# Kernel tuning notes

Hardware: AMD Instinct MI355X
Metric: run time of the kernel (lower is better)

## Reference

```python
import jax, jax.numpy as jnp
import numpy as np

N_NODES = 50000
N_EDGES = 640000
N_GRAPHS = 256
H = 128
L = 4
X_DIM, P_DIM, E_DIM = 64, 16, 16


def setup_inputs() -> dict:
    key = jax.random.key(0)
    ks = jax.random.split(key, 16)
    s = 0.05
    inp = {
        "x": jax.random.normal(ks[0], (N_NODES, X_DIM), jnp.float32),
        "p": jax.random.normal(ks[1], (N_NODES, P_DIM), jnp.float32),
        "e_attr": jax.random.normal(ks[2], (N_EDGES, E_DIM), jnp.float32),
        "edge_index": jax.random.randint(ks[3], (2, N_EDGES), 0, N_NODES, jnp.int32),
        "batch": jnp.sort(jax.random.randint(ks[4], (N_NODES,), 0, N_GRAPHS, jnp.int32)),
        # embeddings
        "W_embed": jax.random.normal(ks[5], (X_DIM + P_DIM, H), jnp.float32) * s,
        "b_embed": jnp.zeros((H,), jnp.float32),
        "W_eembed": jax.random.normal(ks[6], (E_DIM, H), jnp.float32) * s,
        "b_eembed": jnp.zeros((H,), jnp.float32),
        # per-layer stacked params
        "Wm": jax.random.normal(ks[7], (L, 3 * H, H), jnp.float32) * s,
        "bm": jnp.zeros((L, H), jnp.float32),
        "Wh": jax.random.normal(ks[8], (L, 2 * H, H), jnp.float32) * s,
        "bh": jnp.zeros((L, H), jnp.float32),
        "We": jax.random.normal(ks[9], (L, 3 * H, H), jnp.float32) * s,
        "be": jnp.zeros((L, H), jnp.float32),
    }
    return inp


def reference(x, p, e_attr, W_embed, b_embed, W_eembed, b_eembed,
              Wm, bm, Wh, bh, We, be, edge_index, batch):
    # node embed: Linear(cat(x, p))
    h = jnp.concatenate([x, p], axis=1) @ W_embed + b_embed          # [N, H]
    e = e_attr @ W_eembed + b_eembed                                 # [E, H]
    send, rec = edge_index[0], edge_index[1]
    n_nodes = x.shape[0]
    for l in range(Wm.shape[0]):
        h_send, h_rec = h[send], h[rec]                              # gathers [E, H]
        cat_ser = jnp.concatenate([h_send, h_rec, e], axis=1)        # [E, 3H]
        messages = cat_ser @ Wm[l] + bm[l]                           # [E, H]
        messages_agg = jax.ops.segment_sum(messages, rec, num_segments=n_nodes)  # scatter_add
        h = jnp.concatenate([h, messages_agg], axis=1) @ Wh[l] + bh[l]
        # e_update uses h_send/h_rec gathered from the PRE-update h (as in torch code)
        e = cat_ser @ We[l] + be[l]
    # global_add_pool over graphs
    out = jax.ops.segment_sum(h, batch, num_segments=N_GRAPHS)       # [G, H]
    return out
```

## Files before the change

### kernel.cpp

```cpp
#include <hip/hip_runtime.h>
#include <cstdio>

#define NN 50000
#define NE 640000
#define NG 256
#define NL 4

#define SCAN_CHUNK 1024
#define NB_SCAN ((NN + SCAN_CHUNK - 1) / SCAN_CHUNK)

typedef unsigned short u16;
typedef unsigned int u32;
typedef __attribute__((ext_vector_type(8))) short short8v;
typedef __attribute__((ext_vector_type(4))) float f32x4;

static __device__ __forceinline__ float bf2f(u16 v) {
    return __uint_as_float(((u32)v) << 16);
}
static __device__ __forceinline__ u16 f2bf(float f) {
    u32 u = __float_as_uint(f);
    u += 0x7fff + ((u >> 16) & 1);
    return (u16)(u >> 16);
}
static __device__ __forceinline__ void gload_lds16(const u16* g, u16* l) {
    __builtin_amdgcn_global_load_lds(
        (const __attribute__((address_space(1))) u32*)g,
        (__attribute__((address_space(3))) u32*)l, 16, 0, 0);
}

__global__ __launch_bounds__(256) void k_deg(
    const int* __restrict__ rec, int* __restrict__ deg)
{
    const int e = blockIdx.x * 256 + threadIdx.x;
    atomicAdd(&deg[rec[e]], 1);
}

__global__ __launch_bounds__(256) void k_prep_xp(
    const float* __restrict__ x, const float* __restrict__ p,
    u16* __restrict__ Axp)
{
    const int idx = blockIdx.x * 256 + threadIdx.x;
    const int row = idx / 48;
    const int c2 = idx - row * 48;
    const int c0 = c2 * 2;
    float f0, f1;
    if (c0 < 64)      { f0 = x[(size_t)row * 64 + c0]; f1 = x[(size_t)row * 64 + c0 + 1]; }
    else if (c0 < 80) { f0 = p[(size_t)row * 16 + c0 - 64]; f1 = p[(size_t)row * 16 + c0 - 63]; }
    else              { f0 = 0.f; f1 = 0.f; }
    ((u32*)Axp)[idx] = (u32)f2bf(f0) | ((u32)f2bf(f1) << 16);
}

__global__ __launch_bounds__(256) void k_wembed(
    const float* __restrict__ W, u16* __restrict__ Wp)
{
    const int idx = blockIdx.x * 256 + threadIdx.x;
    const int ks = idx >> 12;
    const int rem = idx & 4095;
    const int col = rem >> 5;
    const int kk = rem & 31;
    const int k = ks * 32 + kk;
    Wp[((size_t)ks * 128 + col) * 32 + kk] = f2bf(k < 80 ? W[k * 128 + col] : 0.f);
}

__global__ __launch_bounds__(256) void k_embed(
    const u16* __restrict__ Axp, const u16* __restrict__ Wp,
    const float* __restrict__ b, u16* __restrict__ h)
{
    const int t = threadIdx.x;
    const int lane = t & 63;
    const int w = t >> 6;
    const int rb = blockIdx.x * 128 + w * 32;
    const int l15 = lane & 15;
    const int kg  = lane >> 4;

    int r0 = rb + l15;      if (r0 > NN - 1) r0 = NN - 1;
    int r1 = rb + 16 + l15; if (r1 > NN - 1) r1 = NN - 1;

    f32x4 acc[2][8];
    #pragma unroll
    for (int m = 0; m < 2; ++m)
        #pragma unroll
        for (int n = 0; n < 8; ++n) acc[m][n] = (f32x4){0.f, 0.f, 0.f, 0.f};

    #pragma unroll
    for (int ks = 0; ks < 3; ++ks) {
        const short8v a0 = *(const short8v*)(Axp + (size_t)r0 * 96 + ks * 32 + kg * 8);
        const short8v a1 = *(const short8v*)(Axp + (size_t)r1 * 96 + ks * 32 + kg * 8);
        const u16* bb = Wp + ((size_t)ks * 128 + l15) * 32 + kg * 8;
        #pragma unroll
        for (int nf = 0; nf < 8; ++nf) {
            const short8v bv = *(const short8v*)(bb + (size_t)nf * 16 * 32);
            acc[0][nf] = __builtin_amdgcn_mfma_f32_16x16x32_bf16(a0, bv, acc[0][nf], 0, 0, 0);
            acc[1][nf] = __builtin_amdgcn_mfma_f32_16x16x32_bf16(a1, bv, acc[1][nf], 0, 0, 0);
        }
    }

    #pragma unroll
    for (int m = 0; m < 2; ++m) {
        #pragma unroll
        for (int r = 0; r < 4; ++r) {
            const int row = rb + m * 16 + kg * 4 + r;
            if (row < NN) {
                #pragma unroll
                for (int nf = 0; nf < 8; ++nf) {
                    const int col = nf * 16 + l15;
                    h[(size_t)row * 128 + col] = f2bf(acc[m][nf][r] + b[col]);
                }
            }
        }
    }
}

__global__ __launch_bounds__(256) void k_wprep(
    const float* __restrict__ Wm, const float* __restrict__ Wh,
    const float* __restrict__ We, const float* __restrict__ bm,
    float* __restrict__ Wb, float* __restrict__ cvec)
{
    const int idx = blockIdx.x * 256 + threadIdx.x;
    const int total = 4 * 512 * 256;
    if (idx < total) {
        const int l = idx >> 17;
        const int rem = idx & 131071;
        const int k = rem >> 8;
        const int c = rem & 255;
        const float* Wm_l = Wm + (size_t)l * 384 * 128;
        const float* Wh_l = Wh + (size_t)l * 256 * 128;
        const float* We_l = We + (size_t)l * 384 * 128;
        float v;
        if (k < 128) {
            v = (c < 128) ? Wh_l[k * 128 + c] : 0.f;
        } else {
            const int kk  = (k - 128) & 127;
            const int blk = (k - 128) >> 7;
            const int roff = (blk == 0) ? 128 : (blk == 1) ? 0 : 256;
            if (c < 128) {
                float s = 0.f;
                #pragma unroll 4
                for (int j = 0; j < 128; ++j)
                    s += Wm_l[(roff + kk) * 128 + j] * Wh_l[(128 + j) * 128 + c];
                v = s;
            } else {
                v = We_l[(roff + kk) * 128 + (c - 128)];
            }
        }
        Wb[idx] = v;
    } else if (idx < total + 512) {
        const int r = idx - total;
        const int l = r >> 7;
        const int c = r & 127;
        const float* Wh_l = Wh + (size_t)l * 256 * 128;
        const float* bm_l = bm + l * 128;
        float s = 0.f;
        #pragma unroll 4
        for (int j = 0; j < 128; ++j) s += bm_l[j] * Wh_l[(128 + j) * 128 + c];
        cvec[r] = s;
    }
}

__global__ __launch_bounds__(256) void k_wswz(
    const float* __restrict__ Wb, u16* __restrict__ Bp)
{
    const int idx = blockIdx.x * 256 + threadIdx.x;
    const int l = idx >> 17;
    const int rem = idx & 131071;
    const int k = rem >> 8;
    const int n = rem & 255;
    const int ks = k >> 5;
    const int kg = (k >> 3) & 3;
    const int kk = k & 7;
    Bp[(size_t)l * 131072 + (((size_t)ks * 4 + kg) * 256 + n) * 8 + kk] = f2bf(Wb[idx]);
}

__global__ __launch_bounds__(256) void k_scanA(
    const int* __restrict__ deg, int* __restrict__ part)
{
    __shared__ int red[256];
    const int t = threadIdx.x;
    const int base = blockIdx.x * SCAN_CHUNK + t * 4;
    int s = 0;
    #pragma unroll
    for (int i = 0; i < 4; ++i) {
        const int idx = base + i;
        if (idx < NN) s += deg[idx];
    }
    red[t] = s;
    __syncthreads();
    for (int off = 128; off > 0; off >>= 1) {
        if (t < off) red[t] += red[t + off];
        __syncthreads();
    }
    if (t == 0) part[blockIdx.x] = red[0];
}

__global__ __launch_bounds__(64) void k_scanB(int* part)
{
    if (threadIdx.x == 0) {
        int run = 0;
        for (int b = 0; b < NB_SCAN; ++b) {
            const int v = part[b];
            part[b] = run;
            run += v;
        }
    }
}

__global__ __launch_bounds__(256) void k_scanC(
    const int* __restrict__ deg, const int* __restrict__ part,
    int* __restrict__ offs, int* __restrict__ cursor)
{
    __shared__ int ts[256];
    const int t = threadIdx.x;
    const int base = blockIdx.x * SCAN_CHUNK + t * 4;
    int v[4]; int s = 0;
    #pragma unroll
    for (int i = 0; i < 4; ++i) {
        const int idx = base + i;
        v[i] = (idx < NN) ? deg[idx] : 0;
        s += v[i];
    }
    ts[t] = s;
    __syncthreads();
    for (int off = 1; off < 256; off <<= 1) {
        int val = ts[t];
        if (t >= off) val += ts[t - off];
        __syncthreads();
        ts[t] = val;
        __syncthreads();
    }
    int run = part[blockIdx.x] + ((t == 0) ? 0 : ts[t - 1]);
    #pragma unroll
    for (int i = 0; i < 4; ++i) {
        const int idx = base + i;
        if (idx < NN) { offs[idx] = run; cursor[idx] = run; run += v[i]; }
    }
}

__global__ __launch_bounds__(256) void k_fill(
    const int* __restrict__ send, const int* __restrict__ rec,
    int* __restrict__ cursor, int* __restrict__ csr, int* __restrict__ csr_e)
{
    const int e = blockIdx.x * 256 + threadIdx.x;
    const int r = rec[e];
    const int pos = atomicAdd(&cursor[r], 1);
    csr[pos] = send[e];
    csr_e[pos] = e;
}

__global__ __launch_bounds__(256) void k_sea_se0(
    const float* __restrict__ ea, const int* __restrict__ csr_e,
    const int* __restrict__ offs, const int* __restrict__ deg,
    const float* __restrict__ Wee, const float* __restrict__ bee,
    u16* __restrict__ Se)
{
    __shared__ float sea[4][16];
    const int t = threadIdx.x;
    const int lane = t & 63;
    const int w = t >> 6;
    const int nb = blockIdx.x * 4;
    const int node = nb + w;
    const int g = lane >> 4;
    const int l16 = lane & 15;
    const int off = offs[node];
    const int d = deg[node];

    float acc = 0.f;
    for (int j = g; j < d; j += 4) {
        const int eid = csr_e[off + j];
        acc += ea[(size_t)eid * 16 + l16];
    }
    acc += __shfl_xor(acc, 16);
    acc += __shfl_xor(acc, 32);
    if (g == 0) sea[w][l16] = acc;
    __syncthreads();

    const int c = t & 127;
    #pragma unroll
    for (int q = 0; q < 2; ++q) {
        const int n = (t >> 7) + 2 * q;
        const int nd = nb + n;
        float a = (float)deg[nd] * bee[c];
        #pragma unroll
        for (int k = 0; k < 16; ++k) a += sea[n][k] * Wee[k * 128 + c];
        Se[(size_t)nd * 128 + c] = f2bf(a);
    }
}

__global__ __launch_bounds__(256) void k_gather(
    const u16* __restrict__ h, const int* __restrict__ csr,
    const int* __restrict__ offs, const int* __restrict__ deg,
    u16* __restrict__ Sh)
{
    const int t = threadIdx.x;
    const int lane = t & 63;
    const int node = blockIdx.x * 4 + (t >> 6);
    const int g = lane >> 4;
    const int l16 = lane & 15;
    const int off = offs[node];
    const int d = deg[node];
    const uint4* hp = (const uint4*)h;

    float a[8], b[8];
    #pragma unroll
    for (int i = 0; i < 8; ++i) { a[i] = 0.f; b[i] = 0.f; }

    int j = g;
    for (; j + 4 < d; j += 8) {
        const int s0 = csr[off + j];
        const int s1 = csr[off + j + 4];
        const uint4 v0 = hp[(size_t)s0 * 16 + l16];
        const uint4 v1 = hp[(size_t)s1 * 16 + l16];
        a[0] += bf2f((u16)(v0.x & 0xffff)); a[1] += bf2f((u16)(v0.x >> 16));
        a[2] += bf2f((u16)(v0.y & 0xffff)); a[3] += bf2f((u16)(v0.y >> 16));
        a[4] += bf2f((u16)(v0.z & 0xffff)); a[5] += bf2f((u16)(v0.z >> 16));
        a[6] += bf2f((u16)(v0.w & 0xffff)); a[7] += bf2f((u16)(v0.w >> 16));
        b[0] += bf2f((u16)(v1.x & 0xffff)); b[1] += bf2f((u16)(v1.x >> 16));
        b[2] += bf2f((u16)(v1.y & 0xffff)); b[3] += bf2f((u16)(v1.y >> 16));
        b[4] += bf2f((u16)(v1.z & 0xffff)); b[5] += bf2f((u16)(v1.z >> 16));
        b[6] += bf2f((u16)(v1.w & 0xffff)); b[7] += bf2f((u16)(v1.w >> 16));
    }
    if (j < d) {
        const uint4 v0 = hp[(size_t)csr[off + j] * 16 + l16];
        a[0] += bf2f((u16)(v0.x & 0xffff)); a[1] += bf2f((u16)(v0.x >> 16));
        a[2] += bf2f((u16)(v0.y & 0xffff)); a[3] += bf2f((u16)(v0.y >> 16));
        a[4] += bf2f((u16)(v0.z & 0xffff)); a[5] += bf2f((u16)(v0.z >> 16));
        a[6] += bf2f((u16)(v0.w & 0xffff)); a[7] += bf2f((u16)(v0.w >> 16));
    }
    #pragma unroll
    for (int i = 0; i < 8; ++i) {
        float s = a[i] + b[i];
        s += __shfl_xor(s, 16);
        s += __shfl_xor(s, 32);
        a[i] = s;
    }
    if (g == 0) {
        uint4 o;
        o.x = (u32)f2bf(a[0]) | ((u32)f2bf(a[1]) << 16);
        o.y = (u32)f2bf(a[2]) | ((u32)f2bf(a[3]) << 16);
        o.z = (u32)f2bf(a[4]) | ((u32)f2bf(a[5]) << 16);
        o.w = (u32)f2bf(a[6]) | ((u32)f2bf(a[7]) << 16);
        ((uint4*)Sh)[(size_t)node * 16 + l16] = o;
    }
}

template<bool FULL>
__global__ __launch_bounds__(256) void k_dense(
    const u16* __restrict__ h, const u16* __restrict__ Sh,
    const u16* __restrict__ Se, const int* __restrict__ deg,
    const u16* __restrict__ Bp, const float* __restrict__ cvec,
    const float* __restrict__ bh, const float* __restrict__ be,
    u16* __restrict__ h_out, u16* __restrict__ Se_out)
{
    __shared__ u16 Bs[2][8192];
    const int t = threadIdx.x;
    const int lane = t & 63;
    const int w = t >> 6;
    const int cb = w * 64;
    const int rb = blockIdx.x * 32;
    const int l15 = lane & 15;
    const int kg  = lane >> 4;

    int r0 = rb + l15;      if (r0 > NN - 1) r0 = NN - 1;
    int r1 = rb + 16 + l15; if (r1 > NN - 1) r1 = NN - 1;

    #define STAGE(buf, ks)                                                  \
        {                                                                   \
            const u16* src = Bp + (size_t)(ks) * 8192 + t * 8;              \
            u16* dst = &Bs[buf][t * 8];                                     \
            gload_lds16(src,        dst);                                   \
            gload_lds16(src + 2048, dst + 2048);                            \
            gload_lds16(src + 4096, dst + 4096);                            \
            gload_lds16(src + 6144, dst + 6144);                            \
        }

    short8v Ah[2][4];
    f32x4 accP[2][4], accQ[2][4];
    #pragma unroll
    for (int m = 0; m < 2; ++m)
        #pragma unroll
        for (int n = 0; n < 4; ++n) {
            accP[m][n] = (f32x4){0.f, 0.f, 0.f, 0.f};
            accQ[m][n] = (f32x4){0.f, 0.f, 0.f, 0.f};
        }

    STAGE(0, 0)
    __syncthreads();

    #pragma unroll
    for (int ks = 0; ks < 16; ++ks) {
        const int cur = ks & 1;
        if (ks < 15) STAGE(cur ^ 1, ks + 1)

        const int s = ks >> 2;
        const int k4 = ks & 3;
        const int ko = k4 * 32 + kg * 8;

        if (FULL || w < 2) {
            short8v a0, a1;
            if (s == 0) {
                a0 = *(const short8v*)(h + (size_t)r0 * 128 + ko);
                a1 = *(const short8v*)(h + (size_t)r1 * 128 + ko);
                Ah[0][k4] = a0; Ah[1][k4] = a1;
            } else if (s == 1) {
                a0 = Ah[0][k4]; a1 = Ah[1][k4];
            } else if (s == 2) {
                a0 = *(const short8v*)(Sh + (size_t)r0 * 128 + ko);
                a1 = *(const short8v*)(Sh + (size_t)r1 * 128 + ko);
            } else {
                a0 = *(const short8v*)(Se + (size_t)r0 * 128 + ko);
                a1 = *(const short8v*)(Se + (size_t)r1 * 128 + ko);
            }

            const u16* bs = &Bs[cur][((size_t)kg * 256 + cb + l15) * 8];
            #pragma unroll
            for (int nf = 0; nf < 4; ++nf) {
                const short8v b = *(const short8v*)(bs + nf * 128);
                if (s == 1) {
                    accQ[0][nf] = __builtin_amdgcn_mfma_f32_16x16x32_bf16(a0, b, accQ[0][nf], 0, 0, 0);
                    accQ[1][nf] = __builtin_amdgcn_mfma_f32_16x16x32_bf16(a1, b, accQ[1][nf], 0, 0, 0);
                } else {
                    accP[0][nf] = __builtin_amdgcn_mfma_f32_16x16x32_bf16(a0, b, accP[0][nf], 0, 0, 0);
                    accP[1][nf] = __builtin_amdgcn_mfma_f32_16x16x32_bf16(a1, b, accP[1][nf], 0, 0, 0);
                }
            }
        }
        __syncthreads();
    }
    #undef STAGE

    if (!FULL && w >= 2) return;

    #pragma unroll
    for (int m = 0; m < 2; ++m) {
        #pragma unroll
        for (int r = 0; r < 4; ++r) {
            const int row = rb + m * 16 + kg * 4 + r;
            if (row < NN) {
                const float dg = (float)deg[row];
                if (cb < 128) {
                    #pragma unroll
                    for (int nf = 0; nf < 4; ++nf) {
                        const int col = cb + nf * 16 + l15;
                        h_out[(size_t)row * 128 + col] =
                            f2bf(accP[m][nf][r] + dg * accQ[m][nf][r] + bh[col] + dg * cvec[col]);
                    }
                } else {
                    #pragma unroll
                    for (int nf = 0; nf < 4; ++nf) {
                        const int col = cb - 128 + nf * 16 + l15;
                        Se_out[(size_t)row * 128 + col] =
                            f2bf(accP[m][nf][r] + dg * accQ[m][nf][r] + dg * be[col]);
                    }
                }
            }
        }
    }
}

__global__ __launch_bounds__(256) void k_pool(
    const u16* __restrict__ h, const int* __restrict__ batch,
    float* __restrict__ out)
{
    const int t = threadIdx.x;
    const int col = t & 127;
    const int half = t >> 7;
    const int base = blockIdx.x * 64 + half * 32;
    float acc = 0.f;
    int curg = -1;
    for (int i = 0; i < 32; ++i) {
        const int n = base + i;
        if (n >= NN) break;
        const int g = batch[n];
        if (g != curg) {
            if (curg >= 0) atomicAdd(&out[curg * 128 + col], acc);
            curg = g; acc = 0.f;
        }
        acc += bf2f(h[(size_t)n * 128 + col]);
    }
    if (curg >= 0) atomicAdd(&out[curg * 128 + col], acc);
}

extern "C" void kernel_launch(void* const* d_in, const int* in_sizes, int n_in,
                              void* d_out, int out_size, void* d_ws, size_t ws_size,
                              hipStream_t stream)
{
    const float* x       = (const float*)d_in[0];
    const float* p       = (const float*)d_in[1];
    const float* ea      = (const float*)d_in[2];
    const int*   eidx    = (const int*)d_in[3];
    const int*   batch   = (const int*)d_in[4];
    const float* W_embed = (const float*)d_in[5];
    const float* b_embed = (const float*)d_in[6];
    const float* W_ee    = (const float*)d_in[7];
    const float* b_ee    = (const float*)d_in[8];
    const float* Wm      = (const float*)d_in[9];
    const float* bm      = (const float*)d_in[10];
    const float* Wh      = (const float*)d_in[11];
    const float* bh      = (const float*)d_in[12];
    const float* We      = (const float*)d_in[13];
    const float* be      = (const float*)d_in[14];
    const int* send = eidx;
    const int* rec  = eidx + NE;

    char* w = (char*)d_ws;
    const size_t NHb = (size_t)NN * 128 * sizeof(u16);
    u16* hA  = (u16*)w; w += NHb;
    u16* hB  = (u16*)w; w += NHb;
    u16* SeA = (u16*)w; w += NHb;
    u16* SeB = (u16*)w; w += NHb;
    u16* Sh  = (u16*)w; w += NHb;
    u16* Axp = (u16*)w;  w += (size_t)NN * 96 * 2;
    int*  deg    = (int*)w;   w += (size_t)NN * 4;
    int*  offs   = (int*)w;   w += (size_t)(NN + 4) * 4;
    int*  cursor = (int*)w;   w += (size_t)NN * 4;
    int*  csr    = (int*)w;   w += (size_t)NE * 4;
    int*  csr_e  = (int*)w;   w += (size_t)NE * 4;
    int*  part   = (int*)w;   w += 64 * 4;
    float* Wb    = (float*)w; w += (size_t)4 * 512 * 256 * 4;
    float* cvec  = (float*)w; w += 512 * 4;
    u16*  Bp     = (u16*)w;   w += (size_t)4 * 512 * 256 * 2;
    u16*  Wpe    = (u16*)w;   w += (size_t)3 * 128 * 32 * 2;
    const size_t need = (size_t)(w - (char*)d_ws);
    if (ws_size < need) {
        fprintf(stderr, "[kernel_launch] ws_size=%zu < needed=%zu — skipping\n",
                ws_size, need);
        return;
    }

    float* out = (float*)d_out;

    hipMemsetAsync(d_out, 0, (size_t)NG * 128 * sizeof(float), stream);
    hipMemsetAsync(deg, 0, (size_t)NN * sizeof(int), stream);

    k_deg<<<NE / 256, 256, 0, stream>>>(rec, deg);
    k_prep_xp<<<NN * 48 / 256, 256, 0, stream>>>(x, p, Axp);
    k_wembed<<<3 * 128 * 32 / 256, 256, 0, stream>>>(W_embed, Wpe);
    k_embed<<<(NN + 127) / 128, 256, 0, stream>>>(Axp, Wpe, b_embed, hA);
    k_wprep<<<(4 * 512 * 256 + 512 + 255) / 256, 256, 0, stream>>>(Wm, Wh, We, bm, Wb, cvec);
    k_wswz<<<4 * 512 * 256 / 256, 256, 0, stream>>>(Wb, Bp);
    k_scanA<<<NB_SCAN, 256, 0, stream>>>(deg, part);
    k_scanB<<<1, 64, 0, stream>>>(part);
    k_scanC<<<NB_SCAN, 256, 0, stream>>>(deg, part, offs, cursor);
    k_fill<<<NE / 256, 256, 0, stream>>>(send, rec, cursor, csr, csr_e);
    k_sea_se0<<<NN / 4, 256, 0, stream>>>(ea, csr_e, offs, deg, W_ee, b_ee, SeA);

    u16* h_cur = hA;   u16* h_nxt = hB;
    u16* Se_cur = SeA; u16* Se_nxt = SeB;
    for (int l = 0; l < NL; ++l) {
        k_gather<<<NN / 4, 256, 0, stream>>>(h_cur, csr, offs, deg, Sh);
        if (l < NL - 1)
            k_dense<true><<<(NN + 31) / 32, 256, 0, stream>>>(h_cur, Sh, Se_cur,
                deg, Bp + (size_t)l * 131072,
                cvec + l * 128, bh + l * 128, be + l * 128, h_nxt, Se_nxt);
        else
            k_dense<false><<<(NN + 31) / 32, 256, 0, stream>>>(h_cur, Sh, Se_cur,
                deg, Bp + (size_t)l * 131072,
                cvec + l * 128, bh + l * 128, be + l * 128, h_nxt, Se_nxt);
        u16* tmp;
        tmp = h_cur;  h_cur  = h_nxt;  h_nxt  = tmp;
        tmp = Se_cur; Se_cur = Se_nxt; Se_nxt = tmp;
    }
    k_pool<<<(NN + 63) / 64, 256, 0, stream>>>(h_cur, batch, out);
}
```

Measured before the change: 458.3 us.

## Give each wave a private weight slice in LDS and double rows per block

The weight matrix is re-swizzled so each wave's 64-column slice is contiguous. Each wave now stages only its own slice into a private LDS double buffer, synchronised with explicit waitcnt instead of block-wide __syncthreads. Blocks cover 64 rows instead of 32, so each B fragment feeds four MFMAs and weight staging per row is halved. The cached h operand reuse is dropped: h is reloaded for the second segment. Accumulator registers double, which may lower occupancy, and the hand-written waitcnt ordering is fragile.

```diff
diff --git a/kernel.cpp b/kernel.cpp
--- a/kernel.cpp
+++ b/kernel.cpp
@@ -168,7 +168,10 @@
     const int ks = k >> 5;
     const int kg = (k >> 3) & 3;
     const int kk = k & 7;
-    Bp[(size_t)l * 131072 + (((size_t)ks * 4 + kg) * 256 + n) * 8 + kk] = f2bf(Wb[idx]);
+    const int cg = n >> 6;
+    const int n64 = n & 63;
+    Bp[(size_t)l * 131072 +
+       ((((size_t)ks * 4 + cg) * 4 + kg) * 64 + n64) * 8 + kk] = f2bf(Wb[idx]);
 }
 
 __global__ __launch_bounds__(256) void k_scanA(
@@ -350,32 +353,36 @@
     const float* __restrict__ bh, const float* __restrict__ be,
     u16* __restrict__ h_out, u16* __restrict__ Se_out)
 {
-    __shared__ u16 Bs[2][8192];
+    __shared__ u16 Bs[4][2][2048];
     const int t = threadIdx.x;
     const int lane = t & 63;
     const int w = t >> 6;
+    if (!FULL && w >= 2) return;
     const int cb = w * 64;
-    const int rb = blockIdx.x * 32;
+    const int rb = blockIdx.x * 64;
     const int l15 = lane & 15;
     const int kg  = lane >> 4;
 
-    int r0 = rb + l15;      if (r0 > NN - 1) r0 = NN - 1;
-    int r1 = rb + 16 + l15; if (r1 > NN - 1) r1 = NN - 1;
-
-    #define STAGE(buf, ks)                                                  \
-        {                                                                   \
-            const u16* src = Bp + (size_t)(ks) * 8192 + t * 8;              \
-            u16* dst = &Bs[buf][t * 8];                                     \
-            gload_lds16(src,        dst);                                   \
-            gload_lds16(src + 2048, dst + 2048);                            \
-            gload_lds16(src + 4096, dst + 4096);                            \
-            gload_lds16(src + 6144, dst + 6144);                            \
-        }
-
-    short8v Ah[2][4];
-    f32x4 accP[2][4], accQ[2][4];
-    #pragma unroll
-    for (int m = 0; m < 2; ++m)
+    int rr[4];
+    #pragma unroll
+    for (int m = 0; m < 4; ++m) {
+        rr[m] = rb + m * 16 + l15;
+        if (rr[m] > NN - 1) rr[m] = NN - 1;
+    }
+
+    #define STAGE(buf, ks)                                                   \
+        {                                                                    \
+            const u16* src = Bp + ((size_t)(ks) * 4 + w) * 2048 + lane * 8;  \
+            u16* dst = &Bs[w][buf][lane * 8];                                \
+            gload_lds16(src,        dst);                                    \
+            gload_lds16(src + 512,  dst + 512);                              \
+            gload_lds16(src + 1024, dst + 1024);                             \
+            gload_lds16(src + 1536, dst + 1536);                             \
+        }
+
+    f32x4 accP[4][4], accQ[4][4];
+    #pragma unroll
+    for (int m = 0; m < 4; ++m)
         #pragma unroll
         for (int n = 0; n < 4; ++n) {
             accP[m][n] = (f32x4){0.f, 0.f, 0.f, 0.f};
@@ -383,54 +390,46 @@
         }
 
     STAGE(0, 0)
-    __syncthreads();
 
     #pragma unroll
     for (int ks = 0; ks < 16; ++ks) {
         const int cur = ks & 1;
-        if (ks < 15) STAGE(cur ^ 1, ks + 1)
-
         const int s = ks >> 2;
         const int k4 = ks & 3;
         const int ko = k4 * 32 + kg * 8;
 
-        if (FULL || w < 2) {
-            short8v a0, a1;
-            if (s == 0) {
-                a0 = *(const short8v*)(h + (size_t)r0 * 128 + ko);
-                a1 = *(const short8v*)(h + (size_t)r1 * 128 + ko);
-                Ah[0][k4] = a0; Ah[1][k4] = a1;
-            } else if (s == 1) {
-                a0 = Ah[0][k4]; a1 = Ah[1][k4];
-            } else if (s == 2) {
-                a0 = *(const short8v*)(Sh + (size_t)r0 * 128 + ko);
-                a1 = *(const short8v*)(Sh + (size_t)r1 * 128 + ko);
-            } else {
-                a0 = *(const short8v*)(Se + (size_t)r0 * 128 + ko);
-                a1 = *(const short8v*)(Se + (size_t)r1 * 128 + ko);
+        const u16* __restrict__ Sp = (s <= 1) ? h : (s == 2) ? Sh : Se;
+        short8v a[4];
+        #pragma unroll
+        for (int m = 0; m < 4; ++m)
+            a[m] = *(const short8v*)(Sp + (size_t)rr[m] * 128 + ko);
+
+        if (ks < 15) {
+            asm volatile("s_waitcnt lgkmcnt(0)" ::: "memory");
+            STAGE(cur ^ 1, ks + 1)
+            asm volatile("s_waitcnt vmcnt(4)" ::: "memory");
+        } else {
+            asm volatile("s_waitcnt vmcnt(4)" ::: "memory");
+        }
+        __builtin_amdgcn_sched_barrier(0);
+
+        const u16* bs = &Bs[w][cur][((size_t)kg * 64 + l15) * 8];
+        #pragma unroll
+        for (int nf = 0; nf < 4; ++nf) {
+            const short8v b = *(const short8v*)(bs + nf * 128);
+            #pragma unroll
+            for (int m = 0; m < 4; ++m) {
+                if (s == 1)
+                    accQ[m][nf] = __builtin_amdgcn_mfma_f32_16x16x32_bf16(a[m], b, accQ[m][nf], 0, 0, 0);
+                else
+                    accP[m][nf] = __builtin_amdgcn_mfma_f32_16x16x32_bf16(a[m], b, accP[m][nf], 0, 0, 0);
             }
-
-            const u16* bs = &Bs[cur][((size_t)kg * 256 + cb + l15) * 8];
-            #pragma unroll
-            for (int nf = 0; nf < 4; ++nf) {
-                const short8v b = *(const short8v*)(bs + nf * 128);
-                if (s == 1) {
-                    accQ[0][nf] = __builtin_amdgcn_mfma_f32_16x16x32_bf16(a0, b, accQ[0][nf], 0, 0, 0);
-                    accQ[1][nf] = __builtin_amdgcn_mfma_f32_16x16x32_bf16(a1, b, accQ[1][nf], 0, 0, 0);
-                } else {
-                    accP[0][nf] = __builtin_amdgcn_mfma_f32_16x16x32_bf16(a0, b, accP[0][nf], 0, 0, 0);
-                    accP[1][nf] = __builtin_amdgcn_mfma_f32_16x16x32_bf16(a1, b, accP[1][nf], 0, 0, 0);
-                }
-            }
-        }
-        __syncthreads();
+        }
     }
     #undef STAGE
 
-    if (!FULL && w >= 2) return;
-
-    #pragma unroll
-    for (int m = 0; m < 2; ++m) {
+    #pragma unroll
+    for (int m = 0; m < 4; ++m) {
         #pragma unroll
         for (int r = 0; r < 4; ++r) {
             const int row = rb + m * 16 + kg * 4 + r;
@@ -548,11 +547,11 @@
     for (int l = 0; l < NL; ++l) {
         k_gather<<<NN / 4, 256, 0, stream>>>(h_cur, csr, offs, deg, Sh);
         if (l < NL - 1)
-            k_dense<true><<<(NN + 31) / 32, 256, 0, stream>>>(h_cur, Sh, Se_cur,
+            k_dense<true><<<(NN + 63) / 64, 256, 0, stream>>>(h_cur, Sh, Se_cur,
                 deg, Bp + (size_t)l * 131072,
                 cvec + l * 128, bh + l * 128, be + l * 128, h_nxt, Se_nxt);
         else
-            k_dense<false><<<(NN + 31) / 32, 256, 0, stream>>>(h_cur, Sh, Se_cur,
+            k_dense<false><<<(NN + 63) / 64, 256, 0, stream>>>(h_cur, Sh, Se_cur,
                 deg, Bp + (size_t)l * 131072,
                 cvec + l * 128, bh + l * 128, be + l * 128, h_nxt, Se_nxt);
         u16* tmp;
```

New measurement: 460.5 us. About the same (+0.5%).

## Load dense-kernel weight fragments directly from global, drop LDS staging

Applied to the files above, without the earlier changes.

Rewrites the weight swizzle so each wave's 64-column group is contiguous, and has k_dense read B fragments straight from global memory (L2/L1-cached) instead of double-buffering them through LDS with a barrier each k-step. It removes the per-step __syncthreads, lets non-FULL waves return early, sets a min-blocks occupancy hint, and skips the zero-contributing h-block MFMAs for the edge-output waves. The cost is repeated global/cache reads of the weights by every block instead of a shared LDS copy.

```diff
diff --git a/kernel.cpp b/kernel.cpp
--- a/kernel.cpp
+++ b/kernel.cpp
@@ -21,11 +21,6 @@
     u32 u = __float_as_uint(f);
     u += 0x7fff + ((u >> 16) & 1);
     return (u16)(u >> 16);
-}
-static __device__ __forceinline__ void gload_lds16(const u16* g, u16* l) {
-    __builtin_amdgcn_global_load_lds(
-        (const __attribute__((address_space(1))) u32*)g,
-        (__attribute__((address_space(3))) u32*)l, 16, 0, 0);
 }
 
 __global__ __launch_bounds__(256) void k_deg(
@@ -168,7 +163,10 @@
     const int ks = k >> 5;
     const int kg = (k >> 3) & 3;
     const int kk = k & 7;
-    Bp[(size_t)l * 131072 + (((size_t)ks * 4 + kg) * 256 + n) * 8 + kk] = f2bf(Wb[idx]);
+    const int cg = n >> 6;
+    const int n64 = n & 63;
+    Bp[(size_t)l * 131072 +
+       ((((size_t)ks * 4 + cg) * 4 + kg) * 64 + n64) * 8 + kk] = f2bf(Wb[idx]);
 }
 
 __global__ __launch_bounds__(256) void k_scanA(
@@ -343,18 +341,19 @@
 }
 
 template<bool FULL>
-__global__ __launch_bounds__(256) void k_dense(
+__global__ __launch_bounds__(256, 2) void k_dense(
     const u16* __restrict__ h, const u16* __restrict__ Sh,
     const u16* __restrict__ Se, const int* __restrict__ deg,
     const u16* __restrict__ Bp, const float* __restrict__ cvec,
     const float* __restrict__ bh, const float* __restrict__ be,
     u16* __restrict__ h_out, u16* __restrict__ Se_out)
 {
-    __shared__ u16 Bs[2][8192];
     const int t = threadIdx.x;
     const int lane = t & 63;
     const int w = t >> 6;
+    if (!FULL && w >= 2) return;
     const int cb = w * 64;
+    const bool isH = (cb < 128);
     const int rb = blockIdx.x * 32;
     const int l15 = lane & 15;
     const int kg  = lane >> 4;
@@ -362,17 +361,9 @@
     int r0 = rb + l15;      if (r0 > NN - 1) r0 = NN - 1;
     int r1 = rb + 16 + l15; if (r1 > NN - 1) r1 = NN - 1;
 
-    #define STAGE(buf, ks)                                                  \
-        {                                                                   \
-            const u16* src = Bp + (size_t)(ks) * 8192 + t * 8;              \
-            u16* dst = &Bs[buf][t * 8];                                     \
-            gload_lds16(src,        dst);                                   \
-            gload_lds16(src + 2048, dst + 2048);                            \
-            gload_lds16(src + 4096, dst + 4096);                            \
-            gload_lds16(src + 6144, dst + 6144);                            \
-        }
-
-    short8v Ah[2][4];
+    #define BFRAG(ks, nf) (*(const short8v*)(Bp + \
+        ((((size_t)(ks) * 4 + w) * 4 + kg) * 64 + (nf) * 16 + l15) * 8))
+
     f32x4 accP[2][4], accQ[2][4];
     #pragma unroll
     for (int m = 0; m < 2; ++m)
@@ -382,38 +373,42 @@
             accQ[m][n] = (f32x4){0.f, 0.f, 0.f, 0.f};
         }
 
-    STAGE(0, 0)
-    __syncthreads();
+    short8v ah0[4], ah1[4];
 
     #pragma unroll
     for (int ks = 0; ks < 16; ++ks) {
-        const int cur = ks & 1;
-        if (ks < 15) STAGE(cur ^ 1, ks + 1)
-
         const int s = ks >> 2;
         const int k4 = ks & 3;
         const int ko = k4 * 32 + kg * 8;
 
-        if (FULL || w < 2) {
-            short8v a0, a1;
-            if (s == 0) {
+        short8v a0, a1;
+        bool active = true;
+        if (s == 0) {
+            if (isH) {
                 a0 = *(const short8v*)(h + (size_t)r0 * 128 + ko);
                 a1 = *(const short8v*)(h + (size_t)r1 * 128 + ko);
-                Ah[0][k4] = a0; Ah[1][k4] = a1;
-            } else if (s == 1) {
-                a0 = Ah[0][k4]; a1 = Ah[1][k4];
-            } else if (s == 2) {
-                a0 = *(const short8v*)(Sh + (size_t)r0 * 128 + ko);
-                a1 = *(const short8v*)(Sh + (size_t)r1 * 128 + ko);
+                ah0[k4] = a0; ah1[k4] = a1;
             } else {
-                a0 = *(const short8v*)(Se + (size_t)r0 * 128 + ko);
-                a1 = *(const short8v*)(Se + (size_t)r1 * 128 + ko);
+                active = false;
             }
-
-            const u16* bs = &Bs[cur][((size_t)kg * 256 + cb + l15) * 8];
+        } else if (s == 1) {
+            if (isH) { a0 = ah0[k4]; a1 = ah1[k4]; }
+            else {
+                a0 = *(const short8v*)(h + (size_t)r0 * 128 + ko);
+                a1 = *(const short8v*)(h + (size_t)r1 * 128 + ko);
+            }
+        } else if (s == 2) {
+            a0 = *(const short8v*)(Sh + (size_t)r0 * 128 + ko);
+            a1 = *(const short8v*)(Sh + (size_t)r1 * 128 + ko);
+        } else {
+            a0 = *(const short8v*)(Se + (size_t)r0 * 128 + ko);
+            a1 = *(const short8v*)(Se + (size_t)r1 * 128 + ko);
+        }
+
+        if (active) {
             #pragma unroll
             for (int nf = 0; nf < 4; ++nf) {
-                const short8v b = *(const short8v*)(bs + nf * 128);
+                const short8v b = BFRAG(ks, nf);
                 if (s == 1) {
                     accQ[0][nf] = __builtin_amdgcn_mfma_f32_16x16x32_bf16(a0, b, accQ[0][nf], 0, 0, 0);
                     accQ[1][nf] = __builtin_amdgcn_mfma_f32_16x16x32_bf16(a1, b, accQ[1][nf], 0, 0, 0);
@@ -423,11 +418,8 @@
                 }
             }
         }
-        __syncthreads();
-    }
-    #undef STAGE
-
-    if (!FULL && w >= 2) return;
+    }
+    #undef BFRAG
 
     #pragma unroll
     for (int m = 0; m < 2; ++m) {
```

Measured after the change: 429.9 us. -6.2%, faster.
